# Optimization experiments

Hardware: AMD Instinct MI355X
Metric: run time of the kernel (lower is better)

The kernel has to match this reference:

```python
import jax, jax.numpy as jnp
import numpy as np

B, T, H, NB, D, DH = 2, 8192, 16, 32, 1024, 128


def setup_inputs() -> dict:
    key = jax.random.key(0)
    ks = jax.random.split(key, 4)
    theta_path = jax.random.normal(ks[0], (B, T, H, NB), dtype=jnp.float32)
    content_emb = jax.random.normal(ks[1], (B, T, D), dtype=jnp.float32)
    W1 = jax.random.normal(ks[2], (D, DH), dtype=jnp.float32) / np.sqrt(D)
    b1 = jnp.zeros((DH,), dtype=jnp.float32)
    W2 = jax.random.normal(ks[3], (DH, H * NB), dtype=jnp.float32) / np.sqrt(DH)
    b2 = jnp.zeros((H * NB,), dtype=jnp.float32)
    log_Q = jnp.full((H, NB), -3.0, dtype=jnp.float32)  # torch init: full(-3.0)
    log_R = jnp.full((H, NB), 1.0, dtype=jnp.float32)   # torch init: full(1.0)
    return {"theta_path": theta_path, "content_emb": content_emb,
            "W1": W1, "b1": b1, "W2": W2, "b2": b2,
            "log_Q": log_Q, "log_R": log_R}


def _steady_state_K(log_Q, log_R):
    # closed-form scalar DARE: K* = (P+Q)/(P+Q+R), P = (-Q + sqrt(Q^2+4QR))/2
    Q = jnp.exp(log_Q)
    R = jnp.exp(log_R)
    P_post = 0.5 * (-Q + jnp.sqrt(Q * Q + 4.0 * Q * R))
    P_pred = P_post + Q
    return P_pred / (P_pred + R)


def _parallel_affine_scan(nu, K_star):
    # d_t = K * sum_{s<=t} (1-K)^(t-s) nu_s via zero-padded FFT convolution
    b, t, h, nb = nu.shape
    alpha = 1.0 - K_star                                   # (H, NB)
    k_idx = jnp.arange(t, dtype=nu.dtype)
    kernel = K_star[..., None] * (alpha[..., None] ** k_idx)  # (H, NB, T)
    pad_len = 2 * t
    kernel_fft = jnp.fft.rfft(kernel, n=pad_len, axis=-1)     # (H, NB, pad/2+1)
    nu_perm = jnp.transpose(nu, (0, 2, 3, 1))                 # (B, H, NB, T)
    nu_fft = jnp.fft.rfft(nu_perm, n=pad_len, axis=-1)
    conv = jnp.fft.irfft(nu_fft * kernel_fft[None], n=pad_len, axis=-1)[..., :t]
    return jnp.transpose(conv, (0, 3, 1, 2))                  # (B, T, H, NB)


def reference(theta_path, content_emb, W1, b1, W2, b2, log_Q, log_R):
    b, t, h, nb = theta_path.shape
    hid = jax.nn.gelu(content_emb @ W1 + b1, approximate=False)  # exact GELU (torch default)
    z_raw = (hid @ W2 + b2).reshape(b, t, h, nb)
    z = jnp.pi * jnp.tanh(z_raw)
    diff = z - theta_path
    nu = jnp.arctan2(jnp.sin(diff), jnp.cos(diff))  # wrap to (-pi, pi]
    K_star = _steady_state_K(log_Q, log_R)
    d = _parallel_affine_scan(nu, K_star)
    theta_hat = theta_path + d
    return theta_hat, d, K_star
```

## Files before the change

kernel.cpp:

```cpp
#include <hip/hip_runtime.h>
#include <math.h>

#define Bq 2
#define Tq 8192
#define Dq 1024
#define DHq 128
#define HNq 512
#define Mq (Bq*Tq)
#define NELEM ((size_t)Mq*HNq)
#define CHL 16
#define NCHK (Mq/CHL)
#define CH8 8
#define NC8 (Mq/CH8)
#define CPS8 (Tq/CH8)

typedef _Float16 half8 __attribute__((ext_vector_type(8)));
typedef float    f32x4 __attribute__((ext_vector_type(4)));

#define SC_LO  2048.0f
#define ISC_LO 4.8828125e-4f


__device__ __forceinline__ float gelu_exact(float x) {
    return 0.5f * x * (1.0f + erff(x * 0.7071067811865475f));
}

__device__ __forceinline__ float wrap_pi(float d) {
    return fmaf(-6.283185307179586f, rintf(d * 0.15915494309189535f), d);
}

__global__ __launch_bounds__(64) void p0_pack(
    const float* __restrict__ W1, const float* __restrict__ W2,
    const float* __restrict__ lq, const float* __restrict__ lr,
    _Float16* __restrict__ w1h, _Float16* __restrict__ w1l,
    _Float16* __restrict__ w2h, _Float16* __restrict__ w2l,
    float* __restrict__ Karr, float* __restrict__ Aarr,
    float* __restrict__ kout)
{
    const int l = threadIdx.x;
    const int u = blockIdx.x;
    if (u == 384) {
        #pragma unroll
        for (int i = 0; i < 8; ++i) {
            int col = i * 64 + l;
            float Q = expf(lq[col]);
            float R = expf(lr[col]);
            float P = 0.5f * (-Q + sqrtf(fmaf(Q, Q, 4.0f * Q * R)));
            float Pp = P + Q;
            float K = Pp / (Pp + R);
            Karr[col] = K;
            Aarr[col] = 1.0f - K;
            kout[col] = K;
        }
        return;
    }
    const float* W; _Float16 *ph, *pl; int ncols, kt, ct, unit;
    if (u < 256) { unit = u;       kt = unit >> 3; ct = unit & 7;  W = W1; ph = w1h; pl = w1l; ncols = 128; }
    else         { unit = u - 256; kt = unit >> 5; ct = unit & 31; W = W2; ph = w2h; pl = w2l; ncols = 512; }
    const int col = ct * 16 + (l & 15);
    const int k0  = kt * 32 + ((l >> 4) * 8);
    half8 hv, lv;
    #pragma unroll
    for (int j = 0; j < 8; ++j) {
        float x = W[(size_t)(k0 + j) * ncols + col];
        _Float16 h = (_Float16)x;
        hv[j] = h;
        lv[j] = (_Float16)((x - (float)h) * SC_LO);
    }
    size_t off = ((size_t)unit * 64 + l) * 8;
    *(half8*)(ph + off) = hv;
    *(half8*)(pl + off) = lv;
}

__global__ __launch_bounds__(256, 4) void k1_mfma(
    const float* __restrict__ A, const _Float16* __restrict__ w1h,
    const _Float16* __restrict__ w1l, const float* __restrict__ b1,
    _Float16* __restrict__ hidH, _Float16* __restrict__ hidL)
{
    __shared__ float ldsR[16 * 132];
    const int tid = threadIdx.x;
    const int w = tid >> 6, l = tid & 63;
    const int lrow = l & 15, lq = l >> 4;
    const int kh = w >> 1, ns = w & 1;
    const int row = blockIdx.x * 16 + lrow;

    f32x4 accM[4] = {};
    f32x4 accC[4] = {};
    const float* ap = A + (size_t)row * Dq + kh * 512 + lq * 8;

    f32x4 a0 = *(const f32x4*)(ap);
    f32x4 a1 = *(const f32x4*)(ap + 4);

    for (int step = 0; step < 16; ++step) {
        f32x4 n0, n1;
        if (step < 15) {
            n0 = *(const f32x4*)(ap + (step + 1) * 32);
            n1 = *(const f32x4*)(ap + (step + 1) * 32 + 4);
        }
        half8 ah, alo;
        {
            float xs[8] = {a0[0], a0[1], a0[2], a0[3], a1[0], a1[1], a1[2], a1[3]};
            #pragma unroll
            for (int j = 0; j < 8; ++j) {
                _Float16 h = (_Float16)xs[j];
                ah[j]  = h;
                alo[j] = (_Float16)((xs[j] - (float)h) * SC_LO);
            }
        }
        const int ktG = kh * 16 + step;
        #pragma unroll
        for (int ct = 0; ct < 4; ++ct) {
            const int ctG = ns * 4 + ct;
            size_t boff = ((size_t)(ktG * 8 + ctG) * 64 + l) * 8;
            const half8 bh = *(const half8*)(w1h + boff);
            const half8 bl = *(const half8*)(w1l + boff);
            accM[ct] = __builtin_amdgcn_mfma_f32_16x16x32_f16(ah,  bh, accM[ct], 0, 0, 0);
            accC[ct] = __builtin_amdgcn_mfma_f32_16x16x32_f16(ah,  bl, accC[ct], 0, 0, 0);
            accC[ct] = __builtin_amdgcn_mfma_f32_16x16x32_f16(alo, bh, accC[ct], 0, 0, 0);
        }
        a0 = n0; a1 = n1;
    }

    if (kh == 0) {
        #pragma unroll
        for (int ct = 0; ct < 4; ++ct) {
            const int ctG = ns * 4 + ct;
            #pragma unroll
            for (int r = 0; r < 4; ++r)
                ldsR[(lq * 4 + r) * 132 + ctG * 16 + lrow] =
                    fmaf(accC[ct][r], ISC_LO, accM[ct][r]);
        }
    }
    __syncthreads();
    if (kh == 1) {
        #pragma unroll
        for (int ct = 0; ct < 4; ++ct) {
            const int ctG = ns * 4 + ct;
            #pragma unroll
            for (int r = 0; r < 4; ++r)
                ldsR[(lq * 4 + r) * 132 + ctG * 16 + lrow] +=
                    fmaf(accC[ct][r], ISC_LO, accM[ct][r]);
        }
    }
    __syncthreads();

    const int kt = w;
    const int dh0 = kt * 32 + lq * 8;
    const float* rp = ldsR + lrow * 132 + dh0;
    f32x4 s0 = *(const f32x4*)rp;
    f32x4 s1 = *(const f32x4*)(rp + 4);
    f32x4 bb0 = *(const f32x4*)(b1 + dh0);
    f32x4 bb1 = *(const f32x4*)(b1 + dh0 + 4);
    half8 hv, lv;
    #pragma unroll
    for (int j = 0; j < 4; ++j) {
        float g = gelu_exact(s0[j] + bb0[j]);
        _Float16 h = (_Float16)g;
        hv[j] = h; lv[j] = (_Float16)((g - (float)h) * SC_LO);
    }
    #pragma unroll
    for (int j = 0; j < 4; ++j) {
        float g = gelu_exact(s1[j] + bb1[j]);
        _Float16 h = (_Float16)g;
        hv[4 + j] = h; lv[4 + j] = (_Float16)((g - (float)h) * SC_LO);
    }
    size_t off = (((size_t)blockIdx.x * 4 + kt) * 64 + l) * 8;
    *(half8*)(hidH + off) = hv;
    *(half8*)(hidL + off) = lv;
}

__global__ __launch_bounds__(256, 4) void k2a_mfma(
    const _Float16* __restrict__ hidH, const _Float16* __restrict__ hidL,
    const _Float16* __restrict__ w2h, const _Float16* __restrict__ w2l,
    const float* __restrict__ b2, const float* __restrict__ theta,
    const float* __restrict__ Karr, const float* __restrict__ Aarr,
    float* __restrict__ nuG, float* __restrict__ carries8)
{
    __shared__ float nuL[16][516];
    const int tid = threadIdx.x;
    const int w = tid >> 6, l = tid & 63;
    const int lrow = l & 15, lq = l >> 4;
    const int blk = blockIdx.x;

    f32x4 accM[8] = {};
    f32x4 accC[8] = {};
    #pragma unroll
    for (int kt = 0; kt < 4; ++kt) {
        size_t aoff = (((size_t)blk * 4 + kt) * 64 + l) * 8;
        const half8 ah  = *(const half8*)(hidH + aoff);
        const half8 alo = *(const half8*)(hidL + aoff);
        #pragma unroll
        for (int ct = 0; ct < 8; ++ct) {
            const int ctG = w * 8 + ct;
            size_t boff = (((size_t)kt * 32 + ctG) * 64 + l) * 8;
            const half8 bh = *(const half8*)(w2h + boff);
            const half8 bl = *(const half8*)(w2l + boff);
            accM[ct] = __builtin_amdgcn_mfma_f32_16x16x32_f16(ah,  bh, accM[ct], 0, 0, 0);
            accC[ct] = __builtin_amdgcn_mfma_f32_16x16x32_f16(ah,  bl, accC[ct], 0, 0, 0);
            accC[ct] = __builtin_amdgcn_mfma_f32_16x16x32_f16(alo, bh, accC[ct], 0, 0, 0);
        }
    }

    const float PI_F = 3.14159265358979323846f;
    #pragma unroll
    for (int ct = 0; ct < 8; ++ct) {
        const int col = w * 128 + ct * 16 + lrow;
        const float bb = b2[col];
        #pragma unroll
        for (int r = 0; r < 4; ++r) {
            const int row = blk * 16 + lq * 4 + r;
            float z = fmaf(accC[ct][r], ISC_LO, accM[ct][r]) + bb;
            float t = PI_F * tanhf(z);
            size_t io = (size_t)row * HNq + col;
            accM[ct][r] = wrap_pi(t - theta[io]);
        }
    }
    #pragma unroll
    for (int ct = 0; ct < 8; ++ct)
        #pragma unroll
        for (int r = 0; r < 4; ++r)
            nuL[lq * 4 + r][w * 128 + ct * 16 + lrow] = accM[ct][r];
    __syncthreads();

    #pragma unroll
    for (int cc = 0; cc < 2; ++cc) {
        const int col = tid + cc * 256;
        const float K = Karr[col], al = Aarr[col];
        #pragma unroll
        for (int sub = 0; sub < 2; ++sub) {
            float c = 0.0f;
            #pragma unroll
            for (int r = 0; r < 8; ++r)
                c = fmaf(al, c, K * nuL[sub * 8 + r][col]);
            carries8[(size_t)(blk * 2 + sub) * HNq + col] = c;
        }
    }
    f32x4* dst = (f32x4*)nuG + (size_t)blk * 2048;
    #pragma unroll
    for (int it = 0; it < 8; ++it) {
        const int g = tid + it * 256;
        const int row = g >> 7, cw = g & 127;
        dst[g] = *(const f32x4*)&nuL[row][cw * 4];
    }
}

__global__ __launch_bounds__(256) void k2b_scan(
    const float* __restrict__ theta, const float* __restrict__ Karr,
    const float* __restrict__ Aarr, const float* __restrict__ carries8,
    float* __restrict__ nud, float* __restrict__ theta_hat)
{
    const int tid = threadIdx.x;
    const int sub = tid >> 7, cg = tid & 127, c0 = cg * 4;
    const int chunk = blockIdx.x * 2 + sub;
    const int cloc = chunk & (CPS8 - 1);
    const int seq0 = chunk - cloc;

    const f32x4 K4 = *(const f32x4*)(Karr + c0);
    const f32x4 A4 = *(const f32x4*)(Aarr + c0);
    f32x4 A8;
    #pragma unroll
    for (int j = 0; j < 4; ++j) {
        float a2 = A4[j] * A4[j];
        float a4 = a2 * a2;
        A8[j] = a4 * a4;
    }
    float amax = fmaxf(fmaxf(A8[0], A8[1]), fmaxf(A8[2], A8[3]));
    int n = cloc;
    if (amax <= 0.0f) {
        n = 0;
    } else {
        float ln = logf(amax);
        if (ln < -1e-9f) {
            int nn = (int)ceilf(-34.0f / ln);
            if (nn < n) n = nn;
        }
    }
    f32x4 s = {0.0f, 0.0f, 0.0f, 0.0f};
    for (int j = cloc - n; j < cloc; ++j) {
        f32x4 cv = *(const f32x4*)(carries8 + (size_t)(seq0 + j) * HNq + c0);
        s = A8 * s + cv;
    }

    const size_t base = (size_t)chunk * CH8 * HNq + c0;
    #pragma unroll
    for (int r = 0; r < CH8; ++r) {
        const size_t idx = base + (size_t)r * HNq;
        f32x4 nu = *(const f32x4*)(nud + idx);
        f32x4 th = *(const f32x4*)(theta + idx);
        s = A4 * s + K4 * nu;
        *(f32x4*)(nud + idx) = s;
        *(f32x4*)(theta_hat + idx) = th + s;
    }
}

extern "C" void kernel_launch(void* const* d_in, const int* in_sizes, int n_in,
                              void* d_out, int out_size, void* d_ws, size_t ws_size,
                              hipStream_t stream) {
    const float* theta   = (const float*)d_in[0];
    const float* content = (const float*)d_in[1];
    const float* W1      = (const float*)d_in[2];
    const float* b1      = (const float*)d_in[3];
    const float* W2      = (const float*)d_in[4];
    const float* b2      = (const float*)d_in[5];
    const float* logQ    = (const float*)d_in[6];
    const float* logR    = (const float*)d_in[7];

    float* out       = (float*)d_out;
    float* theta_hat = out;
    float* dbuf      = out + NELEM;
    float* kout      = out + 2 * NELEM;

    _Float16* w1h  = (_Float16*)d_ws;
    _Float16* w1l  = w1h + 131072;
    _Float16* w2h  = w1l + 131072;
    _Float16* w2l  = w2h + 65536;
    _Float16* hidH = w2l + 65536;
    _Float16* hidL = hidH + 2097152;
    float* Karr    = (float*)(hidL + 2097152);
    float* Aarr    = Karr + 512;
    float* carries8 = Aarr + 512;

    p0_pack<<<dim3(385), 64, 0, stream>>>(W1, W2, logQ, logR,
                                          w1h, w1l, w2h, w2l, Karr, Aarr, kout);
    k1_mfma<<<dim3(Mq / 16), 256, 0, stream>>>(content, w1h, w1l, b1, hidH, hidL);
    k2a_mfma<<<dim3(NCHK), 256, 0, stream>>>(hidH, hidL, w2h, w2l, b2, theta,
                                             Karr, Aarr, dbuf, carries8);
    k2b_scan<<<dim3(NC8 / 2), 256, 0, stream>>>(theta, Karr, Aarr, carries8,
                                                dbuf, theta_hat);
}
```

Measured before the change: 223.5 us.

## Enlarge k1 GEMM tile to 64 rows per block and prefetch W1 fragments

The first GEMM kernel now handles 64 rows per 512-thread block instead of 16 rows per 256-thread block. Each wave computes two 16-row M-tiles, so every loaded W1 hi/lo fragment feeds twice as many MFMAs, and the next step's B fragments are software-prefetched into registers alongside the A prefetch. This cuts redundant W1 traffic and load latency, but raises register pressure (launch bounds 512,2), quadruples LDS use, and leaves fewer blocks to spread across CUs.

```diff
diff --git a/kernel.cpp b/kernel.cpp
--- a/kernel.cpp
+++ b/kernel.cpp
@@ -72,101 +72,134 @@
     *(half8*)(pl + off) = lv;
 }
 
-__global__ __launch_bounds__(256, 4) void k1_mfma(
+__global__ __launch_bounds__(512, 2) void k1_mfma(
     const float* __restrict__ A, const _Float16* __restrict__ w1h,
     const _Float16* __restrict__ w1l, const float* __restrict__ b1,
     _Float16* __restrict__ hidH, _Float16* __restrict__ hidL)
 {
-    __shared__ float ldsR[16 * 132];
+    __shared__ float ldsR[64 * 132];
     const int tid = threadIdx.x;
     const int w = tid >> 6, l = tid & 63;
     const int lrow = l & 15, lq = l >> 4;
-    const int kh = w >> 1, ns = w & 1;
-    const int row = blockIdx.x * 16 + lrow;
-
-    f32x4 accM[4] = {};
-    f32x4 accC[4] = {};
-    const float* ap = A + (size_t)row * Dq + kh * 512 + lq * 8;
-
-    f32x4 a0 = *(const f32x4*)(ap);
-    f32x4 a1 = *(const f32x4*)(ap + 4);
+    const int mg = w >> 2;
+    const int kh = (w >> 1) & 1;
+    const int ns = w & 1;
+    const int rowb = blockIdx.x * 64 + mg * 32;
+
+    f32x4 accM[2][4] = {};
+    f32x4 accC[2][4] = {};
+    const float* ap0 = A + (size_t)(rowb + lrow) * Dq + kh * 512 + lq * 8;
+    const float* ap1 = ap0 + (size_t)16 * Dq;
+
+    f32x4 a0[2], a1[2];
+    a0[0] = *(const f32x4*)(ap0); a1[0] = *(const f32x4*)(ap0 + 4);
+    a0[1] = *(const f32x4*)(ap1); a1[1] = *(const f32x4*)(ap1 + 4);
+
+    half8 bhc[4], blc[4];
+    #pragma unroll
+    for (int ct = 0; ct < 4; ++ct) {
+        size_t boff = ((size_t)((kh * 16) * 8 + ns * 4 + ct) * 64 + l) * 8;
+        bhc[ct] = *(const half8*)(w1h + boff);
+        blc[ct] = *(const half8*)(w1l + boff);
+    }
 
     for (int step = 0; step < 16; ++step) {
-        f32x4 n0, n1;
+        f32x4 n0[2], n1[2];
+        half8 bhn[4], bln[4];
         if (step < 15) {
-            n0 = *(const f32x4*)(ap + (step + 1) * 32);
-            n1 = *(const f32x4*)(ap + (step + 1) * 32 + 4);
-        }
-        half8 ah, alo;
-        {
-            float xs[8] = {a0[0], a0[1], a0[2], a0[3], a1[0], a1[1], a1[2], a1[3]};
-            #pragma unroll
-            for (int j = 0; j < 8; ++j) {
-                _Float16 h = (_Float16)xs[j];
-                ah[j]  = h;
-                alo[j] = (_Float16)((xs[j] - (float)h) * SC_LO);
-            }
-        }
-        const int ktG = kh * 16 + step;
-        #pragma unroll
-        for (int ct = 0; ct < 4; ++ct) {
-            const int ctG = ns * 4 + ct;
-            size_t boff = ((size_t)(ktG * 8 + ctG) * 64 + l) * 8;
-            const half8 bh = *(const half8*)(w1h + boff);
-            const half8 bl = *(const half8*)(w1l + boff);
-            accM[ct] = __builtin_amdgcn_mfma_f32_16x16x32_f16(ah,  bh, accM[ct], 0, 0, 0);
-            accC[ct] = __builtin_amdgcn_mfma_f32_16x16x32_f16(ah,  bl, accC[ct], 0, 0, 0);
-            accC[ct] = __builtin_amdgcn_mfma_f32_16x16x32_f16(alo, bh, accC[ct], 0, 0, 0);
-        }
-        a0 = n0; a1 = n1;
+            n0[0] = *(const f32x4*)(ap0 + (step + 1) * 32);
+            n1[0] = *(const f32x4*)(ap0 + (step + 1) * 32 + 4);
+            n0[1] = *(const f32x4*)(ap1 + (step + 1) * 32);
+            n1[1] = *(const f32x4*)(ap1 + (step + 1) * 32 + 4);
+            const int ktG = kh * 16 + step + 1;
+            #pragma unroll
+            for (int ct = 0; ct < 4; ++ct) {
+                size_t boff = ((size_t)(ktG * 8 + ns * 4 + ct) * 64 + l) * 8;
+                bhn[ct] = *(const half8*)(w1h + boff);
+                bln[ct] = *(const half8*)(w1l + boff);
+            }
+        }
+        #pragma unroll
+        for (int mi = 0; mi < 2; ++mi) {
+            half8 ah, alo;
+            {
+                float xs[8] = {a0[mi][0], a0[mi][1], a0[mi][2], a0[mi][3],
+                               a1[mi][0], a1[mi][1], a1[mi][2], a1[mi][3]};
+                #pragma unroll
+                for (int j = 0; j < 8; ++j) {
+                    _Float16 h = (_Float16)xs[j];
+                    ah[j]  = h;
+                    alo[j] = (_Float16)((xs[j] - (float)h) * SC_LO);
+                }
+            }
+            #pragma unroll
+            for (int ct = 0; ct < 4; ++ct) {
+                accM[mi][ct] = __builtin_amdgcn_mfma_f32_16x16x32_f16(ah,  bhc[ct], accM[mi][ct], 0, 0, 0);
+                accC[mi][ct] = __builtin_amdgcn_mfma_f32_16x16x32_f16(ah,  blc[ct], accC[mi][ct], 0, 0, 0);
+                accC[mi][ct] = __builtin_amdgcn_mfma_f32_16x16x32_f16(alo, bhc[ct], accC[mi][ct], 0, 0, 0);
+            }
+        }
+        a0[0] = n0[0]; a1[0] = n1[0];
+        a0[1] = n0[1]; a1[1] = n1[1];
+        #pragma unroll
+        for (int ct = 0; ct < 4; ++ct) { bhc[ct] = bhn[ct]; blc[ct] = bln[ct]; }
     }
 
     if (kh == 0) {
         #pragma unroll
-        for (int ct = 0; ct < 4; ++ct) {
-            const int ctG = ns * 4 + ct;
-            #pragma unroll
-            for (int r = 0; r < 4; ++r)
-                ldsR[(lq * 4 + r) * 132 + ctG * 16 + lrow] =
-                    fmaf(accC[ct][r], ISC_LO, accM[ct][r]);
-        }
+        for (int mi = 0; mi < 2; ++mi)
+            #pragma unroll
+            for (int ct = 0; ct < 4; ++ct) {
+                const int ctG = ns * 4 + ct;
+                #pragma unroll
+                for (int r = 0; r < 4; ++r)
+                    ldsR[(mg * 32 + mi * 16 + lq * 4 + r) * 132 + ctG * 16 + lrow] =
+                        fmaf(accC[mi][ct][r], ISC_LO, accM[mi][ct][r]);
+            }
     }
     __syncthreads();
     if (kh == 1) {
         #pragma unroll
-        for (int ct = 0; ct < 4; ++ct) {
-            const int ctG = ns * 4 + ct;
-            #pragma unroll
-            for (int r = 0; r < 4; ++r)
-                ldsR[(lq * 4 + r) * 132 + ctG * 16 + lrow] +=
-                    fmaf(accC[ct][r], ISC_LO, accM[ct][r]);
-        }
+        for (int mi = 0; mi < 2; ++mi)
+            #pragma unroll
+            for (int ct = 0; ct < 4; ++ct) {
+                const int ctG = ns * 4 + ct;
+                #pragma unroll
+                for (int r = 0; r < 4; ++r)
+                    ldsR[(mg * 32 + mi * 16 + lq * 4 + r) * 132 + ctG * 16 + lrow] +=
+                        fmaf(accC[mi][ct][r], ISC_LO, accM[mi][ct][r]);
+            }
     }
     __syncthreads();
 
-    const int kt = w;
-    const int dh0 = kt * 32 + lq * 8;
-    const float* rp = ldsR + lrow * 132 + dh0;
-    f32x4 s0 = *(const f32x4*)rp;
-    f32x4 s1 = *(const f32x4*)(rp + 4);
-    f32x4 bb0 = *(const f32x4*)(b1 + dh0);
-    f32x4 bb1 = *(const f32x4*)(b1 + dh0 + 4);
-    half8 hv, lv;
-    #pragma unroll
-    for (int j = 0; j < 4; ++j) {
-        float g = gelu_exact(s0[j] + bb0[j]);
-        _Float16 h = (_Float16)g;
-        hv[j] = h; lv[j] = (_Float16)((g - (float)h) * SC_LO);
-    }
-    #pragma unroll
-    for (int j = 0; j < 4; ++j) {
-        float g = gelu_exact(s1[j] + bb1[j]);
-        _Float16 h = (_Float16)g;
-        hv[4 + j] = h; lv[4 + j] = (_Float16)((g - (float)h) * SC_LO);
-    }
-    size_t off = (((size_t)blockIdx.x * 4 + kt) * 64 + l) * 8;
-    *(half8*)(hidH + off) = hv;
-    *(half8*)(hidL + off) = lv;
+    #pragma unroll
+    for (int uh = 0; uh < 2; ++uh) {
+        const int u  = w + uh * 8;
+        const int cl = u >> 2;
+        const int kt = u & 3;
+        const int dh0 = kt * 32 + lq * 8;
+        const float* rp = ldsR + (cl * 16 + lrow) * 132 + dh0;
+        f32x4 s0 = *(const f32x4*)rp;
+        f32x4 s1 = *(const f32x4*)(rp + 4);
+        f32x4 bb0 = *(const f32x4*)(b1 + dh0);
+        f32x4 bb1 = *(const f32x4*)(b1 + dh0 + 4);
+        half8 hv, lv;
+        #pragma unroll
+        for (int j = 0; j < 4; ++j) {
+            float g = gelu_exact(s0[j] + bb0[j]);
+            _Float16 h = (_Float16)g;
+            hv[j] = h; lv[j] = (_Float16)((g - (float)h) * SC_LO);
+        }
+        #pragma unroll
+        for (int j = 0; j < 4; ++j) {
+            float g = gelu_exact(s1[j] + bb1[j]);
+            _Float16 h = (_Float16)g;
+            hv[4 + j] = h; lv[4 + j] = (_Float16)((g - (float)h) * SC_LO);
+        }
+        size_t off = (((size_t)(blockIdx.x * 4 + cl) * 4 + kt) * 64 + l) * 8;
+        *(half8*)(hidH + off) = hv;
+        *(half8*)(hidL + off) = lv;
+    }
 }
 
 __global__ __launch_bounds__(256, 4) void k2a_mfma(
@@ -322,7 +355,7 @@
 
     p0_pack<<<dim3(385), 64, 0, stream>>>(W1, W2, logQ, logR,
                                           w1h, w1l, w2h, w2l, Karr, Aarr, kout);
-    k1_mfma<<<dim3(Mq / 16), 256, 0, stream>>>(content, w1h, w1l, b1, hidH, hidL);
+    k1_mfma<<<dim3(Mq / 64), 512, 0, stream>>>(content, w1h, w1l, b1, hidH, hidL);
     k2a_mfma<<<dim3(NCHK), 256, 0, stream>>>(hidH, hidL, w2h, w2l, b2, theta,
                                              Karr, Aarr, dbuf, carries8);
     k2b_scan<<<dim3(NC8 / 2), 256, 0, stream>>>(theta, Karr, Aarr, carries8,
```

Result: faster. 218.1 us (-2.4%).

## Tile k1 GEMM over 64 rows with async global-to-LDS double buffering

Applied to the files above, without the earlier changes.

The first GEMM kernel now handles 64 rows per block instead of 16, so each W1 fragment loaded is reused across four row tiles. Loads of A and W1 go through global_load_lds into a per-wave double-buffered LDS ring, with manual waitcnt and sched barriers to overlap the next stage's loads with the MFMAs. The aim is to cut redundant weight traffic and hide memory latency. In exchange it uses 128KB of LDS per block, limiting occupancy to one block per CU, and the grid shrinks by a factor of four.

```diff
diff --git a/kernel.cpp b/kernel.cpp
--- a/kernel.cpp
+++ b/kernel.cpp
@@ -29,6 +29,12 @@
     return fmaf(-6.283185307179586f, rintf(d * 0.15915494309189535f), d);
 }
 
+__device__ __forceinline__ void gl16(const void* g, void* ldsDst) {
+    __builtin_amdgcn_global_load_lds(
+        (const __attribute__((address_space(1))) unsigned int*)g,
+        (__attribute__((address_space(3))) unsigned int*)ldsDst, 16, 0, 0);
+}
+
 __global__ __launch_bounds__(64) void p0_pack(
     const float* __restrict__ W1, const float* __restrict__ W2,
     const float* __restrict__ lq, const float* __restrict__ lr,
@@ -72,101 +78,146 @@
     *(half8*)(pl + off) = lv;
 }
 
-__global__ __launch_bounds__(256, 4) void k1_mfma(
+__global__ __launch_bounds__(256, 1) void k1_mfma(
     const float* __restrict__ A, const _Float16* __restrict__ w1h,
     const _Float16* __restrict__ w1l, const float* __restrict__ b1,
     _Float16* __restrict__ hidH, _Float16* __restrict__ hidL)
 {
-    __shared__ float ldsR[16 * 132];
+    __shared__ char lds[131072];
     const int tid = threadIdx.x;
     const int w = tid >> 6, l = tid & 63;
     const int lrow = l & 15, lq = l >> 4;
     const int kh = w >> 1, ns = w & 1;
-    const int row = blockIdx.x * 16 + lrow;
-
-    f32x4 accM[4] = {};
-    f32x4 accC[4] = {};
-    const float* ap = A + (size_t)row * Dq + kh * 512 + lq * 8;
-
-    f32x4 a0 = *(const f32x4*)(ap);
-    f32x4 a1 = *(const f32x4*)(ap + 4);
-
-    for (int step = 0; step < 16; ++step) {
-        f32x4 n0, n1;
-        if (step < 15) {
-            n0 = *(const f32x4*)(ap + (step + 1) * 32);
-            n1 = *(const f32x4*)(ap + (step + 1) * 32 + 4);
-        }
-        half8 ah, alo;
-        {
-            float xs[8] = {a0[0], a0[1], a0[2], a0[3], a1[0], a1[1], a1[2], a1[3]};
+    const int rowb = blockIdx.x * 64;
+
+    char* wbase = lds + w * 32768;
+    const float* aLane = A + (size_t)(rowb + lrow) * Dq + kh * 512 + lq * 8;
+
+#define STAGE(slot, s) do {                                                   \
+        char* sb_ = wbase + (slot) * 16384;                                   \
+        _Pragma("unroll")                                                     \
+        for (int mi_ = 0; mi_ < 4; ++mi_) {                                   \
+            _Pragma("unroll")                                                 \
+            for (int hf_ = 0; hf_ < 2; ++hf_)                                 \
+                gl16(aLane + (size_t)mi_ * 16 * Dq + (s) * 32 + hf_ * 4,      \
+                     sb_ + (mi_ * 2 + hf_) * 1024);                           \
+        }                                                                     \
+        const int ktG_ = kh * 16 + (s);                                       \
+        _Pragma("unroll")                                                     \
+        for (int ct_ = 0; ct_ < 4; ++ct_) {                                   \
+            size_t bo_ = ((size_t)(ktG_ * 8 + ns * 4 + ct_) * 64 + l) * 8;    \
+            gl16(w1h + bo_, sb_ + 8192 + (ct_ * 2 + 0) * 1024);               \
+            gl16(w1l + bo_, sb_ + 8192 + (ct_ * 2 + 1) * 1024);               \
+        }                                                                     \
+    } while (0)
+
+    STAGE(0, 0);
+    STAGE(1, 1);
+
+    f32x4 accM[4][4] = {};
+    f32x4 accC[4][4] = {};
+
+    #pragma unroll 2
+    for (int s = 0; s < 16; ++s) {
+        asm volatile("s_waitcnt vmcnt(16)" ::: "memory");
+        __builtin_amdgcn_sched_barrier(0);
+        char* sb = wbase + (s & 1) * 16384;
+        f32x4 av[4][2];
+        half8 bh[4], bl[4];
+        #pragma unroll
+        for (int mi = 0; mi < 4; ++mi) {
+            av[mi][0] = *(const f32x4*)(sb + (mi * 2 + 0) * 1024 + l * 16);
+            av[mi][1] = *(const f32x4*)(sb + (mi * 2 + 1) * 1024 + l * 16);
+        }
+        #pragma unroll
+        for (int ct = 0; ct < 4; ++ct) {
+            bh[ct] = *(const half8*)(sb + 8192 + (ct * 2 + 0) * 1024 + l * 16);
+            bl[ct] = *(const half8*)(sb + 8192 + (ct * 2 + 1) * 1024 + l * 16);
+        }
+        asm volatile("s_waitcnt lgkmcnt(0)" ::: "memory");
+        __builtin_amdgcn_sched_barrier(0);
+        int sp = s + 2; if (sp > 15) sp = 15;
+        STAGE(s & 1, sp);
+
+        #pragma unroll
+        for (int mi = 0; mi < 4; ++mi) {
+            half8 ah, alo;
+            {
+                float xs[8] = {av[mi][0][0], av[mi][0][1], av[mi][0][2], av[mi][0][3],
+                               av[mi][1][0], av[mi][1][1], av[mi][1][2], av[mi][1][3]};
+                #pragma unroll
+                for (int j = 0; j < 8; ++j) {
+                    _Float16 h = (_Float16)xs[j];
+                    ah[j]  = h;
+                    alo[j] = (_Float16)((xs[j] - (float)h) * SC_LO);
+                }
+            }
             #pragma unroll
-            for (int j = 0; j < 8; ++j) {
-                _Float16 h = (_Float16)xs[j];
-                ah[j]  = h;
-                alo[j] = (_Float16)((xs[j] - (float)h) * SC_LO);
+            for (int ct = 0; ct < 4; ++ct) {
+                accM[mi][ct] = __builtin_amdgcn_mfma_f32_16x16x32_f16(ah,  bh[ct], accM[mi][ct], 0, 0, 0);
+                accC[mi][ct] = __builtin_amdgcn_mfma_f32_16x16x32_f16(ah,  bl[ct], accC[mi][ct], 0, 0, 0);
+                accC[mi][ct] = __builtin_amdgcn_mfma_f32_16x16x32_f16(alo, bh[ct], accC[mi][ct], 0, 0, 0);
             }
         }
-        const int ktG = kh * 16 + step;
-        #pragma unroll
-        for (int ct = 0; ct < 4; ++ct) {
-            const int ctG = ns * 4 + ct;
-            size_t boff = ((size_t)(ktG * 8 + ctG) * 64 + l) * 8;
-            const half8 bh = *(const half8*)(w1h + boff);
-            const half8 bl = *(const half8*)(w1l + boff);
-            accM[ct] = __builtin_amdgcn_mfma_f32_16x16x32_f16(ah,  bh, accM[ct], 0, 0, 0);
-            accC[ct] = __builtin_amdgcn_mfma_f32_16x16x32_f16(ah,  bl, accC[ct], 0, 0, 0);
-            accC[ct] = __builtin_amdgcn_mfma_f32_16x16x32_f16(alo, bh, accC[ct], 0, 0, 0);
-        }
-        a0 = n0; a1 = n1;
-    }
-
+    }
+#undef STAGE
+
+    float* ldsR = (float*)lds;
+    __syncthreads();
     if (kh == 0) {
         #pragma unroll
-        for (int ct = 0; ct < 4; ++ct) {
-            const int ctG = ns * 4 + ct;
+        for (int mi = 0; mi < 4; ++mi)
             #pragma unroll
-            for (int r = 0; r < 4; ++r)
-                ldsR[(lq * 4 + r) * 132 + ctG * 16 + lrow] =
-                    fmaf(accC[ct][r], ISC_LO, accM[ct][r]);
-        }
+            for (int ct = 0; ct < 4; ++ct) {
+                const int ctG = ns * 4 + ct;
+                #pragma unroll
+                for (int r = 0; r < 4; ++r)
+                    ldsR[(mi * 16 + lq * 4 + r) * 132 + ctG * 16 + lrow] =
+                        fmaf(accC[mi][ct][r], ISC_LO, accM[mi][ct][r]);
+            }
     }
     __syncthreads();
     if (kh == 1) {
         #pragma unroll
-        for (int ct = 0; ct < 4; ++ct) {
-            const int ctG = ns * 4 + ct;
+        for (int mi = 0; mi < 4; ++mi)
             #pragma unroll
-            for (int r = 0; r < 4; ++r)
-                ldsR[(lq * 4 + r) * 132 + ctG * 16 + lrow] +=
-                    fmaf(accC[ct][r], ISC_LO, accM[ct][r]);
-        }
+            for (int ct = 0; ct < 4; ++ct) {
+                const int ctG = ns * 4 + ct;
+                #pragma unroll
+                for (int r = 0; r < 4; ++r)
+                    ldsR[(mi * 16 + lq * 4 + r) * 132 + ctG * 16 + lrow] +=
+                        fmaf(accC[mi][ct][r], ISC_LO, accM[mi][ct][r]);
+            }
     }
     __syncthreads();
 
-    const int kt = w;
-    const int dh0 = kt * 32 + lq * 8;
-    const float* rp = ldsR + lrow * 132 + dh0;
-    f32x4 s0 = *(const f32x4*)rp;
-    f32x4 s1 = *(const f32x4*)(rp + 4);
-    f32x4 bb0 = *(const f32x4*)(b1 + dh0);
-    f32x4 bb1 = *(const f32x4*)(b1 + dh0 + 4);
-    half8 hv, lv;
-    #pragma unroll
-    for (int j = 0; j < 4; ++j) {
-        float g = gelu_exact(s0[j] + bb0[j]);
-        _Float16 h = (_Float16)g;
-        hv[j] = h; lv[j] = (_Float16)((g - (float)h) * SC_LO);
-    }
-    #pragma unroll
-    for (int j = 0; j < 4; ++j) {
-        float g = gelu_exact(s1[j] + bb1[j]);
-        _Float16 h = (_Float16)g;
-        hv[4 + j] = h; lv[4 + j] = (_Float16)((g - (float)h) * SC_LO);
-    }
-    size_t off = (((size_t)blockIdx.x * 4 + kt) * 64 + l) * 8;
-    *(half8*)(hidH + off) = hv;
-    *(half8*)(hidL + off) = lv;
+    #pragma unroll
+    for (int uh = 0; uh < 4; ++uh) {
+        const int cl = w;
+        const int kt = uh;
+        const int dh0 = kt * 32 + lq * 8;
+        const float* rp = ldsR + (cl * 16 + lrow) * 132 + dh0;
+        f32x4 s0 = *(const f32x4*)rp;
+        f32x4 s1 = *(const f32x4*)(rp + 4);
+        f32x4 bb0 = *(const f32x4*)(b1 + dh0);
+        f32x4 bb1 = *(const f32x4*)(b1 + dh0 + 4);
+        half8 hv, lv;
+        #pragma unroll
+        for (int j = 0; j < 4; ++j) {
+            float g = gelu_exact(s0[j] + bb0[j]);
+            _Float16 h = (_Float16)g;
+            hv[j] = h; lv[j] = (_Float16)((g - (float)h) * SC_LO);
+        }
+        #pragma unroll
+        for (int j = 0; j < 4; ++j) {
+            float g = gelu_exact(s1[j] + bb1[j]);
+            _Float16 h = (_Float16)g;
+            hv[4 + j] = h; lv[4 + j] = (_Float16)((g - (float)h) * SC_LO);
+        }
+        size_t off = (((size_t)(blockIdx.x * 4 + cl) * 4 + kt) * 64 + l) * 8;
+        *(half8*)(hidH + off) = hv;
+        *(half8*)(hidL + off) = lv;
+    }
 }
 
 __global__ __launch_bounds__(256, 4) void k2a_mfma(
@@ -322,7 +373,7 @@
 
     p0_pack<<<dim3(385), 64, 0, stream>>>(W1, W2, logQ, logR,
                                           w1h, w1l, w2h, w2l, Karr, Aarr, kout);
-    k1_mfma<<<dim3(Mq / 16), 256, 0, stream>>>(content, w1h, w1l, b1, hidH, hidL);
+    k1_mfma<<<dim3(Mq / 64), 256, 0, stream>>>(content, w1h, w1l, b1, hidH, hidL);
     k2a_mfma<<<dim3(NCHK), 256, 0, stream>>>(hidH, hidL, w2h, w2l, b2, theta,
                                              Karr, Aarr, dbuf, carries8);
     k2b_scan<<<dim3(NC8 / 2), 256, 0, stream>>>(theta, Karr, Aarr, carries8,
```

Measured after the change: 212.2 us. -5.0%, faster.

## Retile first GEMM to 64-row blocks with double-buffered direct-to-LDS loads

Applied to the files above, without the earlier changes.

Rewrites the first projection kernel so each 512-thread block handles 64 rows instead of 16. A and B tiles are staged into swizzled LDS through global_load_lds with two-slot double buffering, so W1 fragments are reused across four row groups rather than each wave reloading them from global memory. The K split across waves is removed and each wave accumulates the full K range in two accumulator sets, and the GELU epilogue is widened to match. This adds two barriers per K step and raises LDS use per block, which lowers occupancy.

```diff
diff --git a/kernel.cpp b/kernel.cpp
--- a/kernel.cpp
+++ b/kernel.cpp
@@ -29,6 +29,12 @@
     return fmaf(-6.283185307179586f, rintf(d * 0.15915494309189535f), d);
 }
 
+__device__ __forceinline__ void gl16(const void* g, void* ldsDst) {
+    __builtin_amdgcn_global_load_lds(
+        (const __attribute__((address_space(1))) unsigned int*)g,
+        (__attribute__((address_space(3))) unsigned int*)ldsDst, 16, 0, 0);
+}
+
 __global__ __launch_bounds__(64) void p0_pack(
     const float* __restrict__ W1, const float* __restrict__ W2,
     const float* __restrict__ lq, const float* __restrict__ lr,
@@ -72,101 +78,131 @@
     *(half8*)(pl + off) = lv;
 }
 
-__global__ __launch_bounds__(256, 4) void k1_mfma(
+__global__ __launch_bounds__(512, 1) void k1_mfma(
     const float* __restrict__ A, const _Float16* __restrict__ w1h,
     const _Float16* __restrict__ w1l, const float* __restrict__ b1,
     _Float16* __restrict__ hidH, _Float16* __restrict__ hidL)
 {
-    __shared__ float ldsR[16 * 132];
+    __shared__ char lds[49152];
     const int tid = threadIdx.x;
     const int w = tid >> 6, l = tid & 63;
     const int lrow = l & 15, lq = l >> 4;
-    const int kh = w >> 1, ns = w & 1;
-    const int row = blockIdx.x * 16 + lrow;
-
-    f32x4 accM[4] = {};
-    f32x4 accC[4] = {};
-    const float* ap = A + (size_t)row * Dq + kh * 512 + lq * 8;
-
-    f32x4 a0 = *(const f32x4*)(ap);
-    f32x4 a1 = *(const f32x4*)(ap + 4);
-
-    for (int step = 0; step < 16; ++step) {
-        f32x4 n0, n1;
-        if (step < 15) {
-            n0 = *(const f32x4*)(ap + (step + 1) * 32);
-            n1 = *(const f32x4*)(ap + (step + 1) * 32 + 4);
-        }
-        half8 ah, alo;
-        {
-            float xs[8] = {a0[0], a0[1], a0[2], a0[3], a1[0], a1[1], a1[2], a1[3]};
-            #pragma unroll
-            for (int j = 0; j < 8; ++j) {
-                _Float16 h = (_Float16)xs[j];
-                ah[j]  = h;
-                alo[j] = (_Float16)((xs[j] - (float)h) * SC_LO);
-            }
-        }
-        const int ktG = kh * 16 + step;
-        #pragma unroll
-        for (int ct = 0; ct < 4; ++ct) {
-            const int ctG = ns * 4 + ct;
-            size_t boff = ((size_t)(ktG * 8 + ctG) * 64 + l) * 8;
-            const half8 bh = *(const half8*)(w1h + boff);
-            const half8 bl = *(const half8*)(w1l + boff);
-            accM[ct] = __builtin_amdgcn_mfma_f32_16x16x32_f16(ah,  bh, accM[ct], 0, 0, 0);
-            accC[ct] = __builtin_amdgcn_mfma_f32_16x16x32_f16(ah,  bl, accC[ct], 0, 0, 0);
-            accC[ct] = __builtin_amdgcn_mfma_f32_16x16x32_f16(alo, bh, accC[ct], 0, 0, 0);
-        }
-        a0 = n0; a1 = n1;
-    }
-
-    if (kh == 0) {
-        #pragma unroll
-        for (int ct = 0; ct < 4; ++ct) {
-            const int ctG = ns * 4 + ct;
-            #pragma unroll
-            for (int r = 0; r < 4; ++r)
-                ldsR[(lq * 4 + r) * 132 + ctG * 16 + lrow] =
-                    fmaf(accC[ct][r], ISC_LO, accM[ct][r]);
-        }
-    }
+    const int rq = w >> 1, ns = w & 1;
+    const int rowb = blockIdx.x * 64;
+
+    const int arow = tid >> 3;
+    const int ac4  = (tid & 7) ^ (arow & 7);
+    const float* aSrc = A + (size_t)(rowb + arow) * Dq + ac4 * 4;
+    const _Float16* bplane = (w & 1) ? w1l : w1h;
+    const _Float16* bSrc0 = bplane + ((size_t)(w >> 1) * 64 + l) * 8;
+    const _Float16* bSrc1 = bplane + ((size_t)(4 + (w >> 1)) * 64 + l) * 8;
+
+#define STAGE(slot, s) do {                                                   \
+        gl16(aSrc + (s) * 32, lds + (slot) * 8192 + w * 1024);                \
+        gl16(bSrc0 + (size_t)(s) * 4096,                                     \
+             lds + 16384 + (slot) * 16384 + w * 1024);                        \
+        gl16(bSrc1 + (size_t)(s) * 4096,                                     \
+             lds + 16384 + (slot) * 16384 + 8192 + w * 1024);                 \
+    } while (0)
+
+    const int aRdRow = (rq * 16 + lrow) * 128;
+    const int aRd0 = ((lq * 2 + 0) ^ (lrow & 7)) * 16;
+    const int aRd1 = ((lq * 2 + 1) ^ (lrow & 7)) * 16;
+    const int ns4 = ns * 4;
+
+    STAGE(0, 0);
+    STAGE(1, 1);
+
+    f32x4 accM[2][4] = {};
+    f32x4 accC[2][4] = {};
+
+#define ITER(s, KH) do {                                                      \
+        asm volatile("s_waitcnt vmcnt(3)" ::: "memory");                      \
+        __builtin_amdgcn_sched_barrier(0);                                    \
+        __builtin_amdgcn_s_barrier();                                         \
+        __builtin_amdgcn_sched_barrier(0);                                    \
+        char* As_ = lds + ((s) & 1) * 8192;                                   \
+        char* Bs_ = lds + 16384 + ((s) & 1) * 16384;                          \
+        f32x4 a0_ = *(const f32x4*)(As_ + aRdRow + aRd0);                     \
+        f32x4 a1_ = *(const f32x4*)(As_ + aRdRow + aRd1);                     \
+        half8 bh_[4], bl_[4];                                                 \
+        _Pragma("unroll")                                                     \
+        for (int ct_ = 0; ct_ < 4; ++ct_) {                                   \
+            bh_[ct_] = *(const half8*)(Bs_ + ((ns4 + ct_) * 2 + 0) * 1024 + l * 16); \
+            bl_[ct_] = *(const half8*)(Bs_ + ((ns4 + ct_) * 2 + 1) * 1024 + l * 16); \
+        }                                                                     \
+        asm volatile("s_waitcnt lgkmcnt(0)" ::: "memory");                    \
+        __builtin_amdgcn_sched_barrier(0);                                    \
+        __builtin_amdgcn_s_barrier();                                         \
+        __builtin_amdgcn_sched_barrier(0);                                    \
+        { int sp_ = (s) + 2; if (sp_ > 31) sp_ = 31; STAGE((s) & 1, sp_); }   \
+        half8 ah_, alo_;                                                      \
+        { float xs_[8] = {a0_[0], a0_[1], a0_[2], a0_[3],                     \
+                          a1_[0], a1_[1], a1_[2], a1_[3]};                    \
+          _Pragma("unroll")                                                   \
+          for (int j_ = 0; j_ < 8; ++j_) {                                    \
+              _Float16 h_ = (_Float16)xs_[j_];                                \
+              ah_[j_]  = h_;                                                  \
+              alo_[j_] = (_Float16)((xs_[j_] - (float)h_) * SC_LO);           \
+          } }                                                                 \
+        _Pragma("unroll")                                                     \
+        for (int ct_ = 0; ct_ < 4; ++ct_) {                                   \
+            accM[KH][ct_] = __builtin_amdgcn_mfma_f32_16x16x32_f16(ah_,  bh_[ct_], accM[KH][ct_], 0, 0, 0); \
+            accC[KH][ct_] = __builtin_amdgcn_mfma_f32_16x16x32_f16(ah_,  bl_[ct_], accC[KH][ct_], 0, 0, 0); \
+            accC[KH][ct_] = __builtin_amdgcn_mfma_f32_16x16x32_f16(alo_, bh_[ct_], accC[KH][ct_], 0, 0, 0); \
+        }                                                                     \
+    } while (0)
+
+    #pragma unroll 2
+    for (int s = 0; s < 16; ++s)  ITER(s, 0);
+    #pragma unroll 2
+    for (int s = 16; s < 32; ++s) ITER(s, 1);
+
+#undef ITER
+#undef STAGE
+
+    asm volatile("s_waitcnt vmcnt(0)" ::: "memory");
     __syncthreads();
-    if (kh == 1) {
-        #pragma unroll
-        for (int ct = 0; ct < 4; ++ct) {
-            const int ctG = ns * 4 + ct;
-            #pragma unroll
-            for (int r = 0; r < 4; ++r)
-                ldsR[(lq * 4 + r) * 132 + ctG * 16 + lrow] +=
-                    fmaf(accC[ct][r], ISC_LO, accM[ct][r]);
-        }
+    float* ldsR = (float*)lds;
+    #pragma unroll
+    for (int ct = 0; ct < 4; ++ct) {
+        const int ctG = ns4 + ct;
+        #pragma unroll
+        for (int r = 0; r < 4; ++r)
+            ldsR[(rq * 16 + lq * 4 + r) * 132 + ctG * 16 + lrow] =
+                fmaf(accC[0][ct][r], ISC_LO, accM[0][ct][r]) +
+                fmaf(accC[1][ct][r], ISC_LO, accM[1][ct][r]);
     }
     __syncthreads();
 
-    const int kt = w;
-    const int dh0 = kt * 32 + lq * 8;
-    const float* rp = ldsR + lrow * 132 + dh0;
-    f32x4 s0 = *(const f32x4*)rp;
-    f32x4 s1 = *(const f32x4*)(rp + 4);
-    f32x4 bb0 = *(const f32x4*)(b1 + dh0);
-    f32x4 bb1 = *(const f32x4*)(b1 + dh0 + 4);
-    half8 hv, lv;
-    #pragma unroll
-    for (int j = 0; j < 4; ++j) {
-        float g = gelu_exact(s0[j] + bb0[j]);
-        _Float16 h = (_Float16)g;
-        hv[j] = h; lv[j] = (_Float16)((g - (float)h) * SC_LO);
-    }
-    #pragma unroll
-    for (int j = 0; j < 4; ++j) {
-        float g = gelu_exact(s1[j] + bb1[j]);
-        _Float16 h = (_Float16)g;
-        hv[4 + j] = h; lv[4 + j] = (_Float16)((g - (float)h) * SC_LO);
-    }
-    size_t off = (((size_t)blockIdx.x * 4 + kt) * 64 + l) * 8;
-    *(half8*)(hidH + off) = hv;
-    *(half8*)(hidL + off) = lv;
+    #pragma unroll
+    for (int uh = 0; uh < 2; ++uh) {
+        const int u  = w * 2 + uh;
+        const int cl = u >> 2;
+        const int kt = u & 3;
+        const int dh0 = kt * 32 + lq * 8;
+        const float* rp = ldsR + (cl * 16 + lrow) * 132 + dh0;
+        f32x4 s0 = *(const f32x4*)rp;
+        f32x4 s1 = *(const f32x4*)(rp + 4);
+        f32x4 bb0 = *(const f32x4*)(b1 + dh0);
+        f32x4 bb1 = *(const f32x4*)(b1 + dh0 + 4);
+        half8 hv, lv;
+        #pragma unroll
+        for (int j = 0; j < 4; ++j) {
+            float g = gelu_exact(s0[j] + bb0[j]);
+            _Float16 h = (_Float16)g;
+            hv[j] = h; lv[j] = (_Float16)((g - (float)h) * SC_LO);
+        }
+        #pragma unroll
+        for (int j = 0; j < 4; ++j) {
+            float g = gelu_exact(s1[j] + bb1[j]);
+            _Float16 h = (_Float16)g;
+            hv[4 + j] = h; lv[4 + j] = (_Float16)((g - (float)h) * SC_LO);
+        }
+        size_t off = (((size_t)(blockIdx.x * 4 + cl) * 4 + kt) * 64 + l) * 8;
+        *(half8*)(hidH + off) = hv;
+        *(half8*)(hidL + off) = lv;
+    }
 }
 
 __global__ __launch_bounds__(256, 4) void k2a_mfma(
@@ -322,7 +358,7 @@
 
     p0_pack<<<dim3(385), 64, 0, stream>>>(W1, W2, logQ, logR,
                                           w1h, w1l, w2h, w2l, Karr, Aarr, kout);
-    k1_mfma<<<dim3(Mq / 16), 256, 0, stream>>>(content, w1h, w1l, b1, hidH, hidL);
+    k1_mfma<<<dim3(Mq / 64), 512, 0, stream>>>(content, w1h, w1l, b1, hidH, hidL);
     k2a_mfma<<<dim3(NCHK), 256, 0, stream>>>(hidH, hidL, w2h, w2l, b2, theta,
                                              Karr, Aarr, dbuf, carries8);
     k2b_scan<<<dim3(NC8 / 2), 256, 0, stream>>>(theta, Karr, Aarr, carries8,
```

New measurement: 209.6 us. 1.07x faster.
